# Optimization experiments

Hardware: AMD Instinct MI355X
Metric: run time of the kernel (lower is better)

The kernel has to match this reference:

```python
import jax, jax.numpy as jnp
import numpy as np

B, N, D = 4, 4096, 1024
H, DH = 16, 64            # num_heads, head dim (D = H*DH)
DFF = 4096
M = 64                    # nb_random_features (support)
EPS_KERN = 1e-6
EPS_LN = 1e-6


def setup_inputs() -> dict:
    key = jax.random.key(0)
    ks = jax.random.split(key, 12)
    s = 0.02
    inp = {
        "x":   jax.random.normal(ks[0], (B, N, D), jnp.float32),
        "Wq":  jax.random.normal(ks[1], (D, H, DH), jnp.float32) * s,
        "Wk":  jax.random.normal(ks[2], (D, H, DH), jnp.float32) * s,
        "Wv":  jax.random.normal(ks[3], (D, H, DH), jnp.float32) * s,
        "Wo":  jax.random.normal(ks[4], (H, DH, D), jnp.float32) * s,
        "proj": jax.random.normal(ks[5], (M, DH), jnp.float32),  # FAVOR+ random projection
        "W1":  jax.random.normal(ks[6], (D, DFF), jnp.float32) * s,
        "b1":  jnp.zeros((DFF,), jnp.float32),
        "W2":  jax.random.normal(ks[7], (DFF, D), jnp.float32) * s,
        "b2":  jnp.zeros((D,), jnp.float32),
        "ln1_g": jnp.ones((D,), jnp.float32),
        "ln1_b": jnp.zeros((D,), jnp.float32),
        "ln2_g": jnp.ones((D,), jnp.float32),
        "ln2_b": jnp.zeros((D,), jnp.float32),
    }
    return inp


def _softmax_kernel_feats(data, proj, is_query):
    # data: [B,N,H,DH], proj: [M,DH] -> features [B,N,H,M] (FAVOR+ softmax kernel)
    dn = 1.0 / jnp.sqrt(jnp.sqrt(jnp.float32(data.shape[-1])))
    ratio = 1.0 / jnp.sqrt(jnp.float32(proj.shape[0]))
    data_dash = jnp.einsum("bnhd,md->bnhm", data * dn, proj)
    diag = jnp.sum(jnp.square(data), axis=-1, keepdims=True) * (dn * dn) / 2.0
    if is_query:
        mx = jnp.max(data_dash, axis=-1, keepdims=True)
    else:
        mx = jnp.max(data_dash)
    return ratio * (jnp.exp(data_dash - diag - mx) + EPS_KERN)


def _layernorm(x, g, b):
    mu = jnp.mean(x, axis=-1, keepdims=True)
    var = jnp.mean(jnp.square(x - mu), axis=-1, keepdims=True)
    return (x - mu) * jax.lax.rsqrt(var + EPS_LN) * g + b


def _encoder_forward(x, Wq, Wk, Wv, Wo, proj, W1, b1, W2, b2, ln1_g, ln1_b, ln2_g, ln2_b):
    q = jnp.einsum("bnd,dhk->bnhk", x, Wq)
    k = jnp.einsum("bnd,dhk->bnhk", x, Wk)
    v = jnp.einsum("bnd,dhk->bnhk", x, Wv)
    qf = _softmax_kernel_feats(q, proj, True)    # [B,N,H,M]
    kf = _softmax_kernel_feats(k, proj, False)   # [B,N,H,M]
    # noncausal linear attention
    kv = jnp.einsum("bnhm,bnhd->bhmd", kf, v)    # [B,H,M,DH]
    num = jnp.einsum("bnhm,bhmd->bnhd", qf, kv)
    den = jnp.einsum("bnhm,bhm->bnh", qf, jnp.sum(kf, axis=1))
    attn = num / den[..., None]                   # [B,N,H,DH]
    attn_out = jnp.einsum("bnhd,hdo->bno", attn, Wo)
    out1 = _layernorm(x + attn_out, ln1_g, ln1_b)
    h = jax.nn.elu(out1 @ W1 + b1)
    ffn_out = h @ W2 + b2
    return _layernorm(out1 + ffn_out, ln2_g, ln2_b)


def reference(x, Wq, Wk, Wv, Wo, proj, W1, b1, W2, b2, ln1_g, ln1_b, ln2_g, ln2_b):
    return _encoder_forward(x, Wq, Wk, Wv, Wo, proj, W1, b1, W2, b2, ln1_g, ln1_b, ln2_g, ln2_b)
```

## Files before the change

### kernel.cpp

```cpp
#include <hip/hip_runtime.h>
#include <math.h>

typedef __attribute__((ext_vector_type(8))) short s16x8;
typedef __attribute__((ext_vector_type(4))) float f32x4;

__device__ __forceinline__ float bf2f(unsigned short u) {
    union { unsigned int i; float f; } c; c.i = ((unsigned int)u) << 16; return c.f;
}
__device__ __forceinline__ unsigned short f2bf(float f) {
    union { float f; unsigned int i; } c; c.f = f;
    unsigned int r = c.i + 0x7fffu + ((c.i >> 16) & 1u);
    return (unsigned short)(r >> 16);
}
__device__ __forceinline__ float wave_sum(float v) {
#pragma unroll
    for (int o = 32; o; o >>= 1) v += __shfl_xor(v, o, 64);
    return v;
}
__device__ __forceinline__ float wave_max(float v) {
#pragma unroll
    for (int o = 32; o; o >>= 1) v = fmaxf(v, __shfl_xor(v, o, 64));
    return v;
}
__device__ __forceinline__ void async_load16(const void* g, void* l) {
    __builtin_amdgcn_global_load_lds(
        (const __attribute__((address_space(1))) unsigned int*)g,
        (__attribute__((address_space(3))) unsigned int*)l, 16, 0, 0);
}

enum { EP_BF16 = 0, EP_ADDF32 = 1, EP_BIAS_ELU_BF16 = 2, EP_QKV = 4, EP_BIAS_ADDBF16 = 5 };

template <int EP>
__global__ __launch_bounds__(256, 2) void gemm_bt(
    const unsigned short* __restrict__ A, int lda,
    const unsigned short* __restrict__ BT, int ldb,
    int K, int ldc,
    float* Cf, unsigned short* Cb,
    const float* __restrict__ bias, const float* addsrc,
    const unsigned short* __restrict__ addb,
    unsigned short* vtout)
{
    __shared__ __align__(16) unsigned short sA[128 * 32];
    __shared__ __align__(16) unsigned short sB[128 * 32];
    const int tid = threadIdx.x;
    const int w = tid >> 6, l = tid & 63;
    const int wm = w & 1, wn = w >> 1;

    unsigned int i = blockIdx.y * gridDim.x + blockIdx.x;
    const unsigned int chunk = (gridDim.x * gridDim.y) >> 3;
    i = (i & 7u) * chunk + (i >> 3);
    const int tileX = i % gridDim.x, tileY = i / gridDim.x;
    const int rowBase = tileY * 128, colBase = tileX * 128;

    f32x4 acc[4][4] = {};

    const int sr = w * 32 + (l >> 2);
    const int sc = (l & 3) * 8;
    const unsigned short* gA0 = A + (size_t)(rowBase + sr) * lda + sc;
    const unsigned short* gA1 = gA0 + (size_t)16 * lda;
    const unsigned short* gB0 = BT + (size_t)(colBase + sr) * ldb + sc;
    const unsigned short* gB1 = gB0 + (size_t)16 * ldb;
    unsigned short* lA0 = sA + (w * 32) * 32;
    unsigned short* lA1 = sA + (w * 32 + 16) * 32;
    unsigned short* lB0 = sB + (w * 32) * 32;
    unsigned short* lB1 = sB + (w * 32 + 16) * 32;

    const int lm = l & 15, lq = l >> 4;
    const int aoff = (wm * 64 + lm) * 32 + lq * 8;
    const int boff = (wn * 64 + lm) * 32 + lq * 8;

    for (int k0 = 0; k0 < K; k0 += 32) {
        __syncthreads();
        async_load16(gA0 + k0, lA0);
        async_load16(gA1 + k0, lA1);
        async_load16(gB0 + k0, lB0);
        async_load16(gB1 + k0, lB1);
        __syncthreads();
        s16x8 af[4], bfr[4];
#pragma unroll
        for (int mi = 0; mi < 4; ++mi) af[mi] = *(const s16x8*)(sA + aoff + mi * 512);
#pragma unroll
        for (int ni = 0; ni < 4; ++ni) bfr[ni] = *(const s16x8*)(sB + boff + ni * 512);
#pragma unroll
        for (int mi = 0; mi < 4; ++mi)
#pragma unroll
            for (int ni = 0; ni < 4; ++ni)
                acc[mi][ni] = __builtin_amdgcn_mfma_f32_16x16x32_bf16(
                    af[mi], bfr[ni], acc[mi][ni], 0, 0, 0);
    }

    if (EP == EP_QKV && colBase >= 2048) {
#pragma unroll
        for (int mi = 0; mi < 4; ++mi) {
            const int row0 = rowBase + wm * 64 + mi * 16 + lq * 4;
            const int bb = row0 >> 12, nn = row0 & 4095;
#pragma unroll
            for (int ni = 0; ni < 4; ++ni) {
                const int c = colBase + wn * 64 + ni * 16 + lm - 2048;
                const int hv = c >> 6, dv = c & 63;
                ushort4 u;
                u.x = f2bf(acc[mi][ni][0]); u.y = f2bf(acc[mi][ni][1]);
                u.z = f2bf(acc[mi][ni][2]); u.w = f2bf(acc[mi][ni][3]);
                *(ushort4*)(vtout + ((size_t)(bb * 16 + hv) * 64 + dv) * 4096 + nn) = u;
            }
        }
    } else {
#pragma unroll
        for (int mi = 0; mi < 4; ++mi) {
            const int r0 = rowBase + wm * 64 + mi * 16 + lq * 4;
#pragma unroll
            for (int ni = 0; ni < 4; ++ni) {
                const int c = colBase + wn * 64 + ni * 16 + lm;
                float bv = 0.f;
                if (EP == EP_BIAS_ELU_BF16 || EP == EP_BIAS_ADDBF16) bv = bias[c];
#pragma unroll
                for (int r = 0; r < 4; ++r) {
                    const size_t idx = (size_t)(r0 + r) * ldc + c;
                    float v = acc[mi][ni][r] + bv;
                    if (EP == EP_ADDF32) v += addsrc[idx];
                    if (EP == EP_BIAS_ADDBF16) v += bf2f(addb[idx]);
                    if (EP == EP_BIAS_ELU_BF16) v = v > 0.f ? v : (expf(v) - 1.f);
                    if (EP == EP_BF16 || EP == EP_BIAS_ELU_BF16 || EP == EP_QKV) Cb[idx] = f2bf(v);
                    else Cf[idx] = v;
                }
            }
        }
    }
}

__global__ __launch_bounds__(256) void transpose_all(
    const float* __restrict__ Wq, const float* __restrict__ Wk,
    const float* __restrict__ Wv, const float* __restrict__ Wo,
    const float* __restrict__ W1, const float* __restrict__ W2,
    unsigned short* WqkvT, unsigned short* WoT,
    unsigned short* W1T, unsigned short* W2T)
{
    __shared__ float t[32][33];
    const int bid = blockIdx.x;
    const float* in;
    unsigned short* out;
    int R, C, tx32, ty32;
    if (bid < 4096) {
        const int job = bid >> 10, tile = bid & 1023;
        ty32 = tile >> 5; tx32 = tile & 31;
        R = 1024; C = 1024;
        if (job == 0)      { in = Wq; out = WqkvT; }
        else if (job == 1) { in = Wk; out = WqkvT + 1024 * 1024; }
        else if (job == 2) { in = Wv; out = WqkvT + 2 * 1024 * 1024; }
        else               { in = Wo; out = WoT; }
    } else if (bid < 8192) {
        const int tile = bid - 4096;
        tx32 = tile & 127; ty32 = tile >> 7;
        R = 1024; C = 4096; in = W1; out = W1T;
    } else {
        const int tile = bid - 8192;
        tx32 = tile & 31; ty32 = tile >> 5;
        R = 4096; C = 1024; in = W2; out = W2T;
    }
    const int c0 = tx32 * 32, r0 = ty32 * 32;
    const int tx = threadIdx.x, ty = threadIdx.y;
#pragma unroll
    for (int j = 0; j < 4; ++j)
        t[ty + j * 8][tx] = in[(size_t)(r0 + ty + j * 8) * C + c0 + tx];
    __syncthreads();
#pragma unroll
    for (int j = 0; j < 4; ++j) {
        int cc = ty + j * 8;
        out[(size_t)(c0 + cc) * R + r0 + tx] = f2bf(t[tx][cc]);
    }
}

__global__ __launch_bounds__(256) void cvt_bf16(const float4* in, ushort4* out) {
    size_t i = (size_t)blockIdx.x * 256 + threadIdx.x;
    float4 v = in[i];
    ushort4 o; o.x = f2bf(v.x); o.y = f2bf(v.y); o.z = f2bf(v.z); o.w = f2bf(v.w);
    out[i] = o;
}

__global__ __launch_bounds__(256, 2) void feat_mfma(
    const unsigned short* __restrict__ qkvb, const float* __restrict__ proj,
    unsigned short* __restrict__ qf, float* __restrict__ kdash,
    float* __restrict__ diagk, float* __restrict__ bmax)
{
    __shared__ __align__(16) unsigned short sQ[8192];
    __shared__ __align__(16) unsigned short sK[8192];
    __shared__ __align__(16) unsigned short sP[4096];
    __shared__ float sdq[128], sdk[128];
    __shared__ float swm[4];
    const int tid = threadIdx.x, w = tid >> 6, l = tid & 63;
    const int t0 = blockIdx.x * 8;
    const int lm = l & 15, lq = l >> 4;

#pragma unroll
    for (int j = 0; j < 4; ++j) {
        const int lt = 2 * w + (j & 1), ks = j >> 1;
        const size_t g = (size_t)(t0 + lt) * 3072 + (l >> 2) * 64 + ks * 32 + (l & 3) * 8;
        async_load16(qkvb + g, sQ + ks * 4096 + lt * 512);
        async_load16(qkvb + g + 1024, sK + ks * 4096 + lt * 512);
    }
    for (int i = tid; i < 4096; i += 256) {
        int m = i >> 6, d = i & 63;
        sP[(d >> 5) * 2048 + m * 32 + (d & 31)] = f2bf(proj[i]);
    }
    __syncthreads();

    {
        int r = tid & 127;
        const unsigned short* src = (tid < 128) ? sQ : sK;
        float s = 0.f;
#pragma unroll
        for (int ks = 0; ks < 2; ++ks) {
            const s16x8* p = (const s16x8*)(src + ks * 4096 + r * 32);
#pragma unroll
            for (int c = 0; c < 4; ++c) {
                s16x8 v = p[c];
#pragma unroll
                for (int e = 0; e < 8; ++e) { float f = bf2f((unsigned short)v[e]); s += f * f; }
            }
        }
        if (tid < 128) sdq[r] = s * 0.0625f; else sdk[r] = s * 0.0625f;
    }
    __syncthreads();

    s16x8 pf2[2][4];
#pragma unroll
    for (int ks = 0; ks < 2; ++ks)
#pragma unroll
        for (int ni = 0; ni < 4; ++ni)
            pf2[ks][ni] = *(const s16x8*)(sP + ks * 2048 + (ni * 16 + lm) * 32 + lq * 8);
    f32x4 qa[2][4] = {}, ka[2][4] = {};
#pragma unroll
    for (int i = 0; i < 2; ++i) {
        const int rowt = (w * 2 + i) * 16 + lm;
#pragma unroll
        for (int ks = 0; ks < 2; ++ks) {
            s16x8 aq = *(const s16x8*)(sQ + ks * 4096 + rowt * 32 + lq * 8);
            s16x8 ak = *(const s16x8*)(sK + ks * 4096 + rowt * 32 + lq * 8);
#pragma unroll
            for (int ni = 0; ni < 4; ++ni) {
                qa[i][ni] = __builtin_amdgcn_mfma_f32_16x16x32_bf16(aq, pf2[ks][ni], qa[i][ni], 0, 0, 0);
                ka[i][ni] = __builtin_amdgcn_mfma_f32_16x16x32_bf16(ak, pf2[ks][ni], ka[i][ni], 0, 0, 0);
            }
        }
    }

    const float dn = 0.35355339059327373f;
    float kmax = -3.0e38f;
#pragma unroll
    for (int i = 0; i < 2; ++i) {
#pragma unroll
        for (int r = 0; r < 4; ++r) {
            const int row = (w * 2 + i) * 16 + lq * 4 + r;
            float q0 = qa[i][0][r] * dn, q1 = qa[i][1][r] * dn;
            float q2 = qa[i][2][r] * dn, q3 = qa[i][3][r] * dn;
            float mq = fmaxf(fmaxf(q0, q1), fmaxf(q2, q3));
#pragma unroll
            for (int o = 1; o < 16; o <<= 1) mq = fmaxf(mq, __shfl_xor(mq, o, 64));
            const float dg = sdq[row];
            const size_t ob = (size_t)t0 * 1024 + (size_t)row * 64 + lm;
            qf[ob]      = f2bf(0.125f * (expf(q0 - dg - mq) + 1e-6f));
            qf[ob + 16] = f2bf(0.125f * (expf(q1 - dg - mq) + 1e-6f));
            qf[ob + 32] = f2bf(0.125f * (expf(q2 - dg - mq) + 1e-6f));
            qf[ob + 48] = f2bf(0.125f * (expf(q3 - dg - mq) + 1e-6f));
#pragma unroll
            for (int ni = 0; ni < 4; ++ni) {
                float kd = ka[i][ni][r] * dn;
                kdash[ob + ni * 16] = kd;
                kmax = fmaxf(kmax, kd);
            }
        }
    }
    kmax = wave_max(kmax);
    if (l == 0) swm[w] = kmax;
    __syncthreads();
    if (tid < 128) diagk[t0 * 16 + tid] = sdk[tid];
    if (tid == 0) bmax[blockIdx.x] = fmaxf(fmaxf(swm[0], swm[1]), fmaxf(swm[2], swm[3]));
}

__global__ __launch_bounds__(256) void max_reduce(const float* bm, float* mx) {
    const int tid = threadIdx.x;
    float m = -3.0e38f;
    for (int i = tid; i < 2048; i += 256) m = fmaxf(m, bm[i]);
    m = wave_max(m);
    __shared__ float s[4];
    if ((tid & 63) == 0) s[tid >> 6] = m;
    __syncthreads();
    if (tid == 0) mx[0] = fmaxf(fmaxf(s[0], s[1]), fmaxf(s[2], s[3]));
}

__global__ __launch_bounds__(256, 2) void kv_fused(
    const float* __restrict__ kdash, const float* __restrict__ diagk,
    const float* __restrict__ mx, const unsigned short* __restrict__ vT,
    float* kv, float* ksum)
{
    __shared__ __align__(16) unsigned short sKF[64 * 72];
    __shared__ __align__(16) unsigned short sV[64 * 72];
    __shared__ float sDiag[1024];
    const int tid = threadIdx.x, w = tid >> 6, l = tid & 63;
    const int bh = blockIdx.x, b = bh >> 4, h = bh & 15;
    const int n0 = blockIdx.y * 1024;
    const int lm = l & 15, lq = l >> 4;
    const float mxv = mx[0];

    for (int i = tid; i < 1024; i += 256)
        sDiag[i] = diagk[(size_t)(b * 4096 + n0 + i) * 16 + h] + mxv;

    s16x8 onesf;
    {
        short ov = (lm == 0) ? (short)0x3F80 : (short)0;
#pragma unroll
        for (int j = 0; j < 8; ++j) onesf[j] = ov;
    }
    f32x4 acc[4] = {};
    f32x4 accS = {};
    __syncthreads();

    for (int c0 = 0; c0 < 1024; c0 += 64) {
        __syncthreads();
        {
            const int n = c0 + l;
            const size_t krow = ((size_t)(b * 4096 + n0 + n)) * 1024 + h * 64 + w * 16;
            const float4* kp = (const float4*)(kdash + krow);
            float4 k0 = kp[0], k1 = kp[1], k2 = kp[2], k3 = kp[3];
            const float dg = sDiag[n];
            float vv[16] = {k0.x, k0.y, k0.z, k0.w, k1.x, k1.y, k1.z, k1.w,
                            k2.x, k2.y, k2.z, k2.w, k3.x, k3.y, k3.z, k3.w};
            unsigned short* dst = sKF + (w * 16) * 72 + l;
#pragma unroll
            for (int e = 0; e < 16; ++e)
                dst[e * 72] = f2bf(0.125f * (expf(vv[e] - dg) + 1e-6f));
        }
        {
            const int d = tid >> 2, nq = tid & 3;
            const uint4* vp = (const uint4*)(vT + ((size_t)bh * 64 + d) * 4096 + n0 + c0 + nq * 16);
            uint4 v0 = vp[0], v1 = vp[1];
            uint4* ldst = (uint4*)(sV + d * 72 + nq * 16);
            ldst[0] = v0; ldst[1] = v1;
        }
        __syncthreads();
#pragma unroll
        for (int ks = 0; ks < 2; ++ks) {
            s16x8 a = *(const s16x8*)(sKF + (w * 16 + lm) * 72 + ks * 32 + lq * 8);
            accS = __builtin_amdgcn_mfma_f32_16x16x32_bf16(a, onesf, accS, 0, 0, 0);
#pragma unroll
            for (int ni = 0; ni < 4; ++ni) {
                s16x8 bf = *(const s16x8*)(sV + (ni * 16 + lm) * 72 + ks * 32 + lq * 8);
                acc[ni] = __builtin_amdgcn_mfma_f32_16x16x32_bf16(a, bf, acc[ni], 0, 0, 0);
            }
        }
    }

    const size_t kvbase = (size_t)bh * 4096;
#pragma unroll
    for (int ni = 0; ni < 4; ++ni)
#pragma unroll
        for (int r = 0; r < 4; ++r)
            atomicAdd(kv + kvbase + (size_t)(w * 16 + lq * 4 + r) * 64 + ni * 16 + lm, acc[ni][r]);
    if (lm == 0)
#pragma unroll
        for (int r = 0; r < 4; ++r)
            atomicAdd(ksum + bh * 64 + w * 16 + lq * 4 + r, accS[r]);
}

__global__ __launch_bounds__(256, 2) void attn_mfma(const unsigned short* __restrict__ qf,
                                                    const float* __restrict__ kv,
                                                    const float* __restrict__ ksum,
                                                    unsigned short* __restrict__ attn) {
    __shared__ __align__(16) unsigned short sA[8192];
    __shared__ __align__(16) unsigned short sB[5120];
    const int tid = threadIdx.x, w = tid >> 6, l = tid & 63;
    const int bh = blockIdx.x, b = bh >> 4, h = bh & 15;
    const int n0 = blockIdx.y * 128;
    const int lm = l & 15, lq = l >> 4;

#pragma unroll
    for (int j = 0; j < 4; ++j) {
        const int r0 = w * 32 + (j & 1) * 16, ks = j >> 1;
        const size_t g = (size_t)(b * 4096 + n0 + r0 + (l >> 2)) * 1024 + h * 64 + ks * 32 + (l & 3) * 8;
        async_load16(qf + g, sA + ks * 4096 + r0 * 32);
    }
    for (int i = tid; i < 5120; i += 256) sB[i] = 0;
    __syncthreads();
    for (int i = tid; i < 4096; i += 256) {
        int m = i >> 6, d = i & 63;
        sB[(m >> 5) * 2560 + d * 32 + (m & 31)] = f2bf(kv[(size_t)bh * 4096 + i]);
    }
    if (tid < 64) {
        int m = tid;
        sB[(m >> 5) * 2560 + 64 * 32 + (m & 31)] = f2bf(ksum[bh * 64 + m]);
    }
    __syncthreads();

    s16x8 bf2r[2][5];
#pragma unroll
    for (int ks = 0; ks < 2; ++ks)
#pragma unroll
        for (int ni = 0; ni < 5; ++ni)
            bf2r[ks][ni] = *(const s16x8*)(sB + ks * 2560 + (ni * 16 + lm) * 32 + lq * 8);
    f32x4 acc[2][5] = {};
#pragma unroll
    for (int i = 0; i < 2; ++i) {
        const int rowt = (w * 2 + i) * 16 + lm;
#pragma unroll
        for (int ks = 0; ks < 2; ++ks) {
            s16x8 a = *(const s16x8*)(sA + ks * 4096 + rowt * 32 + lq * 8);
#pragma unroll
            for (int ni = 0; ni < 5; ++ni)
                acc[i][ni] = __builtin_amdgcn_mfma_f32_16x16x32_bf16(a, bf2r[ks][ni], acc[i][ni], 0, 0, 0);
        }
    }
#pragma unroll
    for (int i = 0; i < 2; ++i) {
#pragma unroll
        for (int r = 0; r < 4; ++r) {
            const int row = (w * 2 + i) * 16 + lq * 4 + r;
            float den = __shfl(acc[i][4][r], l & 48, 64);
            float rd = 1.f / den;
            const size_t ob = (size_t)(b * 4096 + n0 + row) * 1024 + h * 64 + lm;
            attn[ob]      = f2bf(acc[i][0][r] * rd);
            attn[ob + 16] = f2bf(acc[i][1][r] * rd);
            attn[ob + 32] = f2bf(acc[i][2][r] * rd);
            attn[ob + 48] = f2bf(acc[i][3][r] * rd);
        }
    }
}

__device__ __forceinline__ float block_sum256(float v, float* sbuf, int tid) {
    v = wave_sum(v);
    __syncthreads();
    if ((tid & 63) == 0) sbuf[tid >> 6] = v;
    __syncthreads();
    return sbuf[0] + sbuf[1] + sbuf[2] + sbuf[3];
}

template <int WF32, int WBF16>
__global__ __launch_bounds__(256) void ln_kernel(const float* src, const float* g, const float* b,
                                                 float* dstf, unsigned short* dstb) {
    __shared__ float sbuf[4];
    const int t = blockIdx.x, tid = threadIdx.x;
    float4 v = ((const float4*)(src + (size_t)t * 1024))[tid];
    float mu = block_sum256(v.x + v.y + v.z + v.w, sbuf, tid) * (1.f / 1024.f);
    float dx = v.x - mu, dy = v.y - mu, dz = v.z - mu, dw = v.w - mu;
    float var = block_sum256(dx * dx + dy * dy + dz * dz + dw * dw, sbuf, tid) * (1.f / 1024.f);
    float r = rsqrtf(var + 1e-6f);
    float4 gv = ((const float4*)g)[tid];
    float4 bv = ((const float4*)b)[tid];
    float4 o;
    o.x = dx * r * gv.x + bv.x; o.y = dy * r * gv.y + bv.y;
    o.z = dz * r * gv.z + bv.z; o.w = dw * r * gv.w + bv.w;
    if (WF32) ((float4*)(dstf + (size_t)t * 1024))[tid] = o;
    if (WBF16) {
        ushort4 u; u.x = f2bf(o.x); u.y = f2bf(o.y); u.z = f2bf(o.z); u.w = f2bf(o.w);
        ((ushort4*)(dstb + (size_t)t * 1024))[tid] = u;
    }
}

extern "C" void kernel_launch(void* const* d_in, const int* in_sizes, int n_in,
                              void* d_out, int out_size, void* d_ws, size_t ws_size,
                              hipStream_t stream) {
    (void)in_sizes; (void)n_in; (void)out_size; (void)ws_size;
    const float* x    = (const float*)d_in[0];
    const float* Wq   = (const float*)d_in[1];
    const float* Wk   = (const float*)d_in[2];
    const float* Wv   = (const float*)d_in[3];
    const float* Wo   = (const float*)d_in[4];
    const float* proj = (const float*)d_in[5];
    const float* W1   = (const float*)d_in[6];
    const float* b1   = (const float*)d_in[7];
    const float* W2   = (const float*)d_in[8];
    const float* b2   = (const float*)d_in[9];
    const float* g1   = (const float*)d_in[10];
    const float* lb1  = (const float*)d_in[11];
    const float* g2   = (const float*)d_in[12];
    const float* lb2  = (const float*)d_in[13];

    char* ws = (char*)d_ws;
    size_t off = 0;
    auto alloc = [&](size_t bytes) { char* p = ws + off; off += (bytes + 255) & ~(size_t)255; return p; };
    unsigned short* WqkvT = (unsigned short*)alloc((size_t)3072 * 1024 * 2);
    unsigned short* WoT   = (unsigned short*)alloc((size_t)1024 * 1024 * 2);
    unsigned short* W1T   = (unsigned short*)alloc((size_t)4096 * 1024 * 2);
    unsigned short* W2T   = (unsigned short*)alloc((size_t)1024 * 4096 * 2);
    unsigned short* xb    = (unsigned short*)alloc((size_t)16384 * 1024 * 2);
    unsigned short* qkvb  = (unsigned short*)alloc((size_t)16384 * 3072 * 2);
    unsigned short* qf    = (unsigned short*)alloc((size_t)16384 * 1024 * 2);
    unsigned short* vT    = (unsigned short*)alloc((size_t)16384 * 1024 * 2);
    float* kv    = (float*)alloc((size_t)64 * 64 * 64 * 4);
    float* ksum  = (float*)alloc((size_t)64 * 64 * 4);
    float* diagk = (float*)alloc((size_t)16384 * 16 * 4);
    float* bmax  = (float*)alloc((size_t)16384 * 4);
    float* mx    = (float*)alloc(256);

    unsigned short* attnb = xb;
    unsigned short* out1b = qkvb;
    unsigned short* h     = qkvb + (size_t)16384 * 1024;
    float* kdash = (float*)d_out;
    float* preLN = (float*)d_out;

    transpose_all<<<12288, dim3(32, 8), 0, stream>>>(Wq, Wk, Wv, Wo, W1, W2,
                                                     WqkvT, WoT, W1T, W2T);
    cvt_bf16<<<16384, 256, 0, stream>>>((const float4*)x, (ushort4*)xb);

    gemm_bt<EP_QKV><<<dim3(24, 128), 256, 0, stream>>>(xb, 1024, WqkvT, 1024, 1024, 3072,
                                                       nullptr, qkvb, nullptr, nullptr, nullptr, vT);
    feat_mfma<<<2048, 256, 0, stream>>>(qkvb, proj, qf, kdash, diagk, bmax);
    max_reduce<<<1, 256, 0, stream>>>(bmax, mx);
    hipMemsetAsync(kv, 0, (size_t)64 * 64 * 64 * 4 + (size_t)64 * 64 * 4, stream);
    kv_fused<<<dim3(64, 4), 256, 0, stream>>>(kdash, diagk, mx, vT, kv, ksum);
    attn_mfma<<<dim3(64, 32), 256, 0, stream>>>(qf, kv, ksum, attnb);
    gemm_bt<EP_ADDF32><<<dim3(8, 128), 256, 0, stream>>>(attnb, 1024, WoT, 1024, 1024, 1024,
                                                         preLN, nullptr, nullptr, x, nullptr, nullptr);
    ln_kernel<0, 1><<<16384, 256, 0, stream>>>(preLN, g1, lb1, nullptr, out1b);
    gemm_bt<EP_BIAS_ELU_BF16><<<dim3(32, 128), 256, 0, stream>>>(out1b, 1024, W1T, 1024, 1024, 4096,
                                                                 nullptr, h, b1, nullptr, nullptr, nullptr);
    gemm_bt<EP_BIAS_ADDBF16><<<dim3(8, 128), 256, 0, stream>>>(h, 4096, W2T, 4096, 4096, 1024,
                                                               preLN, nullptr, b2, nullptr, out1b, nullptr);
    ln_kernel<1, 0><<<16384, 256, 0, stream>>>(preLN, g2, lb2, (float*)d_out, nullptr);
}
```

Measured before the change: 833.9 us.

## Replace GEMM with 256x256-tile, 512-thread, 4-stage async LDS pipelined kernel

Replaces the 128x128 single-buffered bf16 GEMM with a 256x256 tile kernel run by 8 waves. It uses a 4-slot LDS ring filled by async global-to-LDS loads, with explicit vmcnt waits and one barrier per k-step, so loads overlap the MFMA work. It also raises MFMA priority around the compute and stores LDS in MFMA-fragment order so reads are contiguous. The aim is to remove the two-barrier stall per k-step and improve operand reuse, at the cost of 128KB of LDS per block, lower occupancy, and fewer blocks (wave quantization on 256-CU parts), especially for the N=1024 GEMMs.

Result: slower. 1.016 ms (+21.9%).

```diff
diff --git a/kernel.cpp b/kernel.cpp
--- a/kernel.cpp
+++ b/kernel.cpp
@@ -31,7 +31,7 @@
 enum { EP_BF16 = 0, EP_ADDF32 = 1, EP_BIAS_ELU_BF16 = 2, EP_QKV = 4, EP_BIAS_ADDBF16 = 5 };
 
 template <int EP>
-__global__ __launch_bounds__(256, 2) void gemm_bt(
+__global__ __launch_bounds__(512, 2) void gemm256(
     const unsigned short* __restrict__ A, int lda,
     const unsigned short* __restrict__ BT, int ldb,
     int K, int ldc,
@@ -40,63 +40,89 @@
     const unsigned short* __restrict__ addb,
     unsigned short* vtout)
 {
-    __shared__ __align__(16) unsigned short sA[128 * 32];
-    __shared__ __align__(16) unsigned short sB[128 * 32];
+    __shared__ __align__(16) unsigned short sA[4 * 8192];
+    __shared__ __align__(16) unsigned short sB[4 * 8192];
     const int tid = threadIdx.x;
     const int w = tid >> 6, l = tid & 63;
-    const int wm = w & 1, wn = w >> 1;
+    const int wr = w >> 2, wc = w & 3;
+    const int lm = l & 15, lq = l >> 4;
 
     unsigned int i = blockIdx.y * gridDim.x + blockIdx.x;
     const unsigned int chunk = (gridDim.x * gridDim.y) >> 3;
     i = (i & 7u) * chunk + (i >> 3);
     const int tileX = i % gridDim.x, tileY = i / gridDim.x;
-    const int rowBase = tileY * 128, colBase = tileX * 128;
-
-    f32x4 acc[4][4] = {};
-
-    const int sr = w * 32 + (l >> 2);
-    const int sc = (l & 3) * 8;
-    const unsigned short* gA0 = A + (size_t)(rowBase + sr) * lda + sc;
-    const unsigned short* gA1 = gA0 + (size_t)16 * lda;
-    const unsigned short* gB0 = BT + (size_t)(colBase + sr) * ldb + sc;
-    const unsigned short* gB1 = gB0 + (size_t)16 * ldb;
-    unsigned short* lA0 = sA + (w * 32) * 32;
-    unsigned short* lA1 = sA + (w * 32 + 16) * 32;
-    unsigned short* lB0 = sB + (w * 32) * 32;
-    unsigned short* lB1 = sB + (w * 32 + 16) * 32;
-
-    const int lm = l & 15, lq = l >> 4;
-    const int aoff = (wm * 64 + lm) * 32 + lq * 8;
-    const int boff = (wn * 64 + lm) * 32 + lq * 8;
-
-    for (int k0 = 0; k0 < K; k0 += 32) {
-        __syncthreads();
-        async_load16(gA0 + k0, lA0);
-        async_load16(gA1 + k0, lA1);
-        async_load16(gB0 + k0, lB0);
-        async_load16(gB1 + k0, lB1);
-        __syncthreads();
-        s16x8 af[4], bfr[4];
-#pragma unroll
-        for (int mi = 0; mi < 4; ++mi) af[mi] = *(const s16x8*)(sA + aoff + mi * 512);
-#pragma unroll
-        for (int ni = 0; ni < 4; ++ni) bfr[ni] = *(const s16x8*)(sB + boff + ni * 512);
-#pragma unroll
-        for (int mi = 0; mi < 4; ++mi)
-#pragma unroll
-            for (int ni = 0; ni < 4; ++ni)
-                acc[mi][ni] = __builtin_amdgcn_mfma_f32_16x16x32_bf16(
-                    af[mi], bfr[ni], acc[mi][ni], 0, 0, 0);
-    }
+    const int rowBase = tileY * 256, colBase = tileX * 256;
+
+    f32x4 acc[8][4] = {};
+
+    const unsigned short* gAr0 = A + (size_t)(rowBase + w * 16 + lm) * lda + lq * 8;
+    const unsigned short* gAr1 = A + (size_t)(rowBase + (8 + w) * 16 + lm) * lda + lq * 8;
+    const unsigned short* gBr0 = BT + (size_t)(colBase + w * 16 + lm) * ldb + lq * 8;
+    const unsigned short* gBr1 = BT + (size_t)(colBase + (8 + w) * 16 + lm) * ldb + lq * 8;
+
+#define STAGE_A(J) do { const int _sl = ((J) & 3) * 8192; \
+    async_load16(gAr0 + (size_t)(J) * 32, sA + _sl + w * 512); \
+    async_load16(gAr1 + (size_t)(J) * 32, sA + _sl + (8 + w) * 512); } while (0)
+#define STAGE_B(J) do { const int _sl = ((J) & 3) * 8192; \
+    async_load16(gBr0 + (size_t)(J) * 32, sB + _sl + w * 512); \
+    async_load16(gBr1 + (size_t)(J) * 32, sB + _sl + (8 + w) * 512); } while (0)
+
+#define KSTEP(S) do { \
+    const int _slot = (S) & 3; \
+    const unsigned short* pa = sA + _slot * 8192 + wr * 4096 + l * 8; \
+    const unsigned short* pb = sB + _slot * 8192 + wc * 2048 + l * 8; \
+    s16x8 af[4], bfr[4]; \
+    _Pragma("unroll") for (int n = 0; n < 4; ++n) bfr[n] = *(const s16x8*)(pb + n * 512); \
+    _Pragma("unroll") for (int m = 0; m < 4; ++m) af[m] = *(const s16x8*)(pa + m * 512); \
+    __builtin_amdgcn_s_setprio(1); \
+    _Pragma("unroll") for (int m = 0; m < 4; ++m) \
+    _Pragma("unroll") for (int n = 0; n < 4; ++n) \
+        acc[m][n] = __builtin_amdgcn_mfma_f32_16x16x32_bf16(af[m], bfr[n], acc[m][n], 0, 0, 0); \
+    __builtin_amdgcn_s_setprio(0); \
+    _Pragma("unroll") for (int m = 0; m < 4; ++m) af[m] = *(const s16x8*)(pa + (4 + m) * 512); \
+    __builtin_amdgcn_s_setprio(1); \
+    _Pragma("unroll") for (int m = 0; m < 4; ++m) \
+    _Pragma("unroll") for (int n = 0; n < 4; ++n) \
+        acc[4 + m][n] = __builtin_amdgcn_mfma_f32_16x16x32_bf16(af[m], bfr[n], acc[4 + m][n], 0, 0, 0); \
+    __builtin_amdgcn_s_setprio(0); \
+} while (0)
+
+    const int NK = K >> 5;
+    STAGE_A(0); STAGE_B(0); STAGE_A(1); STAGE_B(1); STAGE_A(2);
+
+    for (int s = 0; s < NK - 3; ++s) {
+        asm volatile("s_waitcnt vmcnt(6)" ::: "memory");
+        __builtin_amdgcn_s_barrier();
+        __builtin_amdgcn_sched_barrier(0);
+        STAGE_B(s + 2); STAGE_A(s + 3);
+        KSTEP(s);
+    }
+    asm volatile("s_waitcnt vmcnt(6)" ::: "memory");
+    __builtin_amdgcn_s_barrier();
+    __builtin_amdgcn_sched_barrier(0);
+    STAGE_B(NK - 1);
+    KSTEP(NK - 3);
+    asm volatile("s_waitcnt vmcnt(4)" ::: "memory");
+    __builtin_amdgcn_s_barrier();
+    __builtin_amdgcn_sched_barrier(0);
+    KSTEP(NK - 2);
+    asm volatile("s_waitcnt vmcnt(0)" ::: "memory");
+    __builtin_amdgcn_s_barrier();
+    __builtin_amdgcn_sched_barrier(0);
+    KSTEP(NK - 1);
+
+#undef STAGE_A
+#undef STAGE_B
+#undef KSTEP
 
     if (EP == EP_QKV && colBase >= 2048) {
 #pragma unroll
-        for (int mi = 0; mi < 4; ++mi) {
-            const int row0 = rowBase + wm * 64 + mi * 16 + lq * 4;
+        for (int mi = 0; mi < 8; ++mi) {
+            const int row0 = rowBase + wr * 128 + mi * 16 + lq * 4;
             const int bb = row0 >> 12, nn = row0 & 4095;
 #pragma unroll
             for (int ni = 0; ni < 4; ++ni) {
-                const int c = colBase + wn * 64 + ni * 16 + lm - 2048;
+                const int c = colBase + wc * 64 + ni * 16 + lm - 2048;
                 const int hv = c >> 6, dv = c & 63;
                 ushort4 u;
                 u.x = f2bf(acc[mi][ni][0]); u.y = f2bf(acc[mi][ni][1]);
@@ -106,11 +132,11 @@
         }
     } else {
 #pragma unroll
-        for (int mi = 0; mi < 4; ++mi) {
-            const int r0 = rowBase + wm * 64 + mi * 16 + lq * 4;
+        for (int mi = 0; mi < 8; ++mi) {
+            const int r0 = rowBase + wr * 128 + mi * 16 + lq * 4;
 #pragma unroll
             for (int ni = 0; ni < 4; ++ni) {
-                const int c = colBase + wn * 64 + ni * 16 + lm;
+                const int c = colBase + wc * 64 + ni * 16 + lm;
                 float bv = 0.f;
                 if (EP == EP_BIAS_ELU_BF16 || EP == EP_BIAS_ADDBF16) bv = bias[c];
 #pragma unroll
@@ -501,19 +527,19 @@
                                                      WqkvT, WoT, W1T, W2T);
     cvt_bf16<<<16384, 256, 0, stream>>>((const float4*)x, (ushort4*)xb);
 
-    gemm_bt<EP_QKV><<<dim3(24, 128), 256, 0, stream>>>(xb, 1024, WqkvT, 1024, 1024, 3072,
-                                                       nullptr, qkvb, nullptr, nullptr, nullptr, vT);
+    gemm256<EP_QKV><<<dim3(12, 64), 512, 0, stream>>>(xb, 1024, WqkvT, 1024, 1024, 3072,
+                                                      nullptr, qkvb, nullptr, nullptr, nullptr, vT);
     feat_mfma<<<2048, 256, 0, stream>>>(qkvb, proj, qf, kdash, diagk, bmax);
     max_reduce<<<1, 256, 0, stream>>>(bmax, mx);
     hipMemsetAsync(kv, 0, (size_t)64 * 64 * 64 * 4 + (size_t)64 * 64 * 4, stream);
     kv_fused<<<dim3(64, 4), 256, 0, stream>>>(kdash, diagk, mx, vT, kv, ksum);
     attn_mfma<<<dim3(64, 32), 256, 0, stream>>>(qf, kv, ksum, attnb);
-    gemm_bt<EP_ADDF32><<<dim3(8, 128), 256, 0, stream>>>(attnb, 1024, WoT, 1024, 1024, 1024,
-                                                         preLN, nullptr, nullptr, x, nullptr, nullptr);
+    gemm256<EP_ADDF32><<<dim3(4, 64), 512, 0, stream>>>(attnb, 1024, WoT, 1024, 1024, 1024,
+                                                        preLN, nullptr, nullptr, x, nullptr, nullptr);
     ln_kernel<0, 1><<<16384, 256, 0, stream>>>(preLN, g1, lb1, nullptr, out1b);
-    gemm_bt<EP_BIAS_ELU_BF16><<<dim3(32, 128), 256, 0, stream>>>(out1b, 1024, W1T, 1024, 1024, 4096,
-                                                                 nullptr, h, b1, nullptr, nullptr, nullptr);
-    gemm_bt<EP_BIAS_ADDBF16><<<dim3(8, 128), 256, 0, stream>>>(h, 4096, W2T, 4096, 4096, 1024,
-                                                               preLN, nullptr, b2, nullptr, out1b, nullptr);
+    gemm256<EP_BIAS_ELU_BF16><<<dim3(16, 64), 512, 0, stream>>>(out1b, 1024, W1T, 1024, 1024, 4096,
+                                                                nullptr, h, b1, nullptr, nullptr, nullptr);
+    gemm256<EP_BIAS_ADDBF16><<<dim3(4, 64), 512, 0, stream>>>(h, 4096, W2T, 4096, 4096, 1024,
+                                                              preLN, nullptr, b2, nullptr, out1b, nullptr);
     ln_kernel<1, 0><<<16384, 256, 0, stream>>>(preLN, g2, lb2, (float*)d_out, nullptr);
 }
```

## Double GEMM K-tile to 64 with XOR-swizzled LDS layout

Applied to the files above, without the earlier changes.

The bf16 GEMM now stages a K-slice of 64 per iteration instead of 32, which halves the number of barrier pairs and load rounds per output tile. The LDS rows are 128 bytes wide and use an XOR swizzle on the 16-byte chunk index, applied on the async global-to-LDS writes and again on the fragment reads, to avoid bank conflicts. LDS use doubles to 32 KB per block, which may reduce occupancy below the two blocks per CU the launch bounds target. K must now be a multiple of 64.

Result: faster. 803.6 us (-3.6%).

```diff
diff --git a/kernel.cpp b/kernel.cpp
--- a/kernel.cpp
+++ b/kernel.cpp
@@ -40,8 +40,8 @@
     const unsigned short* __restrict__ addb,
     unsigned short* vtout)
 {
-    __shared__ __align__(16) unsigned short sA[128 * 32];
-    __shared__ __align__(16) unsigned short sB[128 * 32];
+    __shared__ __align__(16) unsigned short sA[128 * 64];
+    __shared__ __align__(16) unsigned short sB[128 * 64];
     const int tid = threadIdx.x;
     const int w = tid >> 6, l = tid & 63;
     const int wm = w & 1, wn = w >> 1;
@@ -54,39 +54,41 @@
 
     f32x4 acc[4][4] = {};
 
-    const int sr = w * 32 + (l >> 2);
-    const int sc = (l & 3) * 8;
-    const unsigned short* gA0 = A + (size_t)(rowBase + sr) * lda + sc;
-    const unsigned short* gA1 = gA0 + (size_t)16 * lda;
-    const unsigned short* gB0 = BT + (size_t)(colBase + sr) * ldb + sc;
-    const unsigned short* gB1 = gB0 + (size_t)16 * ldb;
-    unsigned short* lA0 = sA + (w * 32) * 32;
-    unsigned short* lA1 = sA + (w * 32 + 16) * 32;
-    unsigned short* lB0 = sB + (w * 32) * 32;
-    unsigned short* lB1 = sB + (w * 32 + 16) * 32;
+    const int lr = l >> 3;
+    const int xs = (l & 7) ^ lr;
+    const unsigned short* gA = A + (size_t)(rowBase + w * 32 + lr) * lda + xs * 8;
+    const unsigned short* gB = BT + (size_t)(colBase + w * 32 + lr) * ldb + xs * 8;
+    unsigned short* lA = sA + (w * 32) * 64;
+    unsigned short* lB = sB + (w * 32) * 64;
 
     const int lm = l & 15, lq = l >> 4;
-    const int aoff = (wm * 64 + lm) * 32 + lq * 8;
-    const int boff = (wn * 64 + lm) * 32 + lq * 8;
-
-    for (int k0 = 0; k0 < K; k0 += 32) {
+    const int lm7 = lm & 7;
+
+    for (int k0 = 0; k0 < K; k0 += 64) {
         __syncthreads();
-        async_load16(gA0 + k0, lA0);
-        async_load16(gA1 + k0, lA1);
-        async_load16(gB0 + k0, lB0);
-        async_load16(gB1 + k0, lB1);
+#pragma unroll
+        for (int j = 0; j < 4; ++j) {
+            async_load16(gA + (size_t)(j * 8) * lda + k0, lA + j * 512);
+            async_load16(gB + (size_t)(j * 8) * ldb + k0, lB + j * 512);
+        }
         __syncthreads();
-        s16x8 af[4], bfr[4];
-#pragma unroll
-        for (int mi = 0; mi < 4; ++mi) af[mi] = *(const s16x8*)(sA + aoff + mi * 512);
-#pragma unroll
-        for (int ni = 0; ni < 4; ++ni) bfr[ni] = *(const s16x8*)(sB + boff + ni * 512);
-#pragma unroll
-        for (int mi = 0; mi < 4; ++mi)
+#pragma unroll
+        for (int kk = 0; kk < 2; ++kk) {
+            const int sl = (((kk << 2) + lq) ^ lm7) * 8;
+            s16x8 af[4], bfr[4];
+#pragma unroll
+            for (int mi = 0; mi < 4; ++mi)
+                af[mi] = *(const s16x8*)(sA + (wm * 64 + mi * 16 + lm) * 64 + sl);
 #pragma unroll
             for (int ni = 0; ni < 4; ++ni)
-                acc[mi][ni] = __builtin_amdgcn_mfma_f32_16x16x32_bf16(
-                    af[mi], bfr[ni], acc[mi][ni], 0, 0, 0);
+                bfr[ni] = *(const s16x8*)(sB + (wn * 64 + ni * 16 + lm) * 64 + sl);
+#pragma unroll
+            for (int mi = 0; mi < 4; ++mi)
+#pragma unroll
+                for (int ni = 0; ni < 4; ++ni)
+                    acc[mi][ni] = __builtin_amdgcn_mfma_f32_16x16x32_bf16(
+                        af[mi], bfr[ni], acc[mi][ni], 0, 0, 0);
+        }
     }
 
     if (EP == EP_QKV && colBase >= 2048) {
```
